# Kernel tuning notes

Hardware: AMD Instinct MI355X
Metric: run time of the kernel (lower is better)

The kernel has to match this reference:

```python
import jax, jax.numpy as jnp
import numpy as np
import math

D_MODEL, D_FF, N_EXPERTS, TOP_K, N_SHARED = 1024, 4096, 8, 2, 1
B, T = 4, 1024
SCALE = 1.0 / math.sqrt(N_SHARED + TOP_K / N_EXPERTS)


def setup_inputs() -> dict:
    key = jax.random.key(0)
    ks = jax.random.split(key, 10)
    s1 = 1.0 / math.sqrt(D_MODEL)
    s2 = 1.0 / math.sqrt(D_FF)
    return {
        "x": jax.random.normal(ks[0], (B, T, D_MODEL), dtype=jnp.float32),
        "w_router": jax.random.normal(ks[1], (N_EXPERTS, D_MODEL), dtype=jnp.float32) * s1,
        "W1": jax.random.normal(ks[2], (N_EXPERTS, D_FF, D_MODEL), dtype=jnp.float32) * s1,
        "b1": jax.random.normal(ks[3], (N_EXPERTS, D_FF), dtype=jnp.float32) * 0.02,
        "W2": jax.random.normal(ks[4], (N_EXPERTS, D_MODEL, D_FF), dtype=jnp.float32) * s2,
        "b2": jax.random.normal(ks[5], (N_EXPERTS, D_MODEL), dtype=jnp.float32) * 0.02,
        "Ws1": jax.random.normal(ks[6], (D_FF, D_MODEL), dtype=jnp.float32) * s1,
        "bs1": jax.random.normal(ks[7], (D_FF,), dtype=jnp.float32) * 0.02,
        "Ws2": jax.random.normal(ks[8], (D_MODEL, D_FF), dtype=jnp.float32) * s2,
        "bs2": jax.random.normal(ks[9], (D_MODEL,), dtype=jnp.float32) * 0.02,
    }


def reference(x, w_router, W1, b1, W2, b2, Ws1, bs1, Ws2, bs2):
    # Router: logits -> softmax -> top-k gate values (no renormalization, matching source)
    logits = jnp.einsum("btd,ed->bte", x, w_router)      # [B,T,E]
    probs = jax.nn.softmax(logits, axis=-1)
    vals, idx = jax.lax.top_k(probs, TOP_K)               # [B,T,K]
    # Scatter top-k gate values into dense per-expert gates [B,T,E]
    gates = jnp.sum(jax.nn.one_hot(idx, N_EXPERTS, dtype=x.dtype) * vals[..., None], axis=-2)

    # Shared (always-on) expert FFN
    hs = jax.nn.gelu(jnp.einsum("btd,fd->btf", x, Ws1) + bs1)
    acc = jnp.einsum("btf,df->btd", hs, Ws2) + bs2

    # Routed experts, densified combine: sum_e gate[b,t,e] * FFN_e(x[b,t])
    h = jax.nn.gelu(jnp.einsum("btd,efd->btef", x, W1) + b1)   # [B,T,E,F]
    y = jnp.einsum("btef,edf->bted", h, W2) + b2               # [B,T,E,D]
    acc = acc + jnp.einsum("bted,bte->btd", y, gates)

    return SCALE * acc
```

## Files before the change

kernel.cpp:

```cpp
#include <hip/hip_runtime.h>
#include <hip/hip_bf16.h>

#define NTOK 4096
#define DM   1024
#define DF   4096
#define ROWS_TOTAL 12288
#define BM 128
#define BN 128
#define BK 64
#define TILES_MAX 112
#define SCALE_F 0.8944271909999159f

typedef __attribute__((ext_vector_type(8))) short short8;
typedef __attribute__((ext_vector_type(4))) float floatx4;

#define GLD16(gp, lp) __builtin_amdgcn_global_load_lds( \
    (const __attribute__((address_space(1))) void*)(gp), \
    (__attribute__((address_space(3))) void*)(lp), 16, 0, 0)

__device__ __forceinline__ ushort f2bf(float f){
    __hip_bfloat16 h = __float2bfloat16(f);
    return *reinterpret_cast<ushort*>(&h);
}

__device__ __forceinline__ float gelu_tanh(float x){
    float u = 0.7978845608028654f * (x + 0.044715f * x * x * x);
    return 0.5f * x * (1.0f + tanhf(u));
}

__global__ __launch_bounds__(256) void cvt_kernel(const float* __restrict__ src,
                                                  ushort* __restrict__ dst, int n4){
    int i = blockIdx.x * 256 + threadIdx.x;
    if (i < n4){
        float4 v = reinterpret_cast<const float4*>(src)[i];
        ushort4 o = { f2bf(v.x), f2bf(v.y), f2bf(v.z), f2bf(v.w) };
        reinterpret_cast<ushort4*>(dst)[i] = o;
    }
}

__global__ __launch_bounds__(256) void router_kernel(
    const float* __restrict__ x, const float* __restrict__ wr,
    int* __restrict__ counts, int* __restrict__ te, float* __restrict__ tg,
    int* __restrict__ tokarr)
{
    const int token = blockIdx.x * 4 + (threadIdx.x >> 6);
    const int lane  = threadIdx.x & 63;
    const float* xp = x + (size_t)token * DM;
    float s[8];
    #pragma unroll
    for (int e = 0; e < 8; e++) s[e] = 0.f;
    for (int d = lane; d < DM; d += 64){
        float xv = xp[d];
        #pragma unroll
        for (int e = 0; e < 8; e++) s[e] += xv * wr[e * DM + d];
    }
    #pragma unroll
    for (int e = 0; e < 8; e++){
        float v = s[e];
        #pragma unroll
        for (int off = 32; off > 0; off >>= 1) v += __shfl_down(v, off);
        s[e] = v;
    }
    if (lane == 0){
        float m = s[0];
        #pragma unroll
        for (int e = 1; e < 8; e++) m = fmaxf(m, s[e]);
        float p[8]; float sum = 0.f;
        #pragma unroll
        for (int e = 0; e < 8; e++){ p[e] = __expf(s[e] - m); sum += p[e]; }
        float inv = 1.f / sum;
        #pragma unroll
        for (int e = 0; e < 8; e++) p[e] *= inv;
        int i1 = 0; float p1 = p[0];
        #pragma unroll
        for (int e = 1; e < 8; e++) if (p[e] > p1){ p1 = p[e]; i1 = e; }
        int i2 = -1; float p2 = -1.f;
        #pragma unroll
        for (int e = 0; e < 8; e++) if (e != i1 && p[e] > p2){ p2 = p[e]; i2 = e; }
        atomicAdd(&counts[i1], 1);
        atomicAdd(&counts[i2], 1);
        te[token*2+0] = i1; te[token*2+1] = i2;
        tg[token*2+0] = p1; tg[token*2+1] = p2;
        tokarr[token] = token;
    }
}

__global__ void scan_kernel(int* counts, int* rowbase, int* cursor, int* tiles){
    if (threadIdx.x == 0 && blockIdx.x == 0){
        int off = NTOK;
        for (int e = 0; e < 8; e++){ rowbase[e] = off; cursor[e] = off; off += counts[e]; }
        rowbase[8] = 0;
        counts[8]  = NTOK;
        int idx = 0;
        for (int e = 0; e < 9; e++){
            int c = counts[e];
            for (int mt = 0; mt * BM < c && idx < TILES_MAX; mt++)
                tiles[idx++] = (e << 8) | mt;
        }
        for (; idx < TILES_MAX; idx++) tiles[idx] = -1;
    }
}

__global__ __launch_bounds__(256) void fill_kernel(
    const int* __restrict__ te, int* cursor, int* tokarr, int* rowof)
{
    int token = blockIdx.x * 256 + threadIdx.x;
    #pragma unroll
    for (int j = 0; j < 2; j++){
        int e = te[token*2+j];
        int p = atomicAdd(&cursor[e], 1);
        tokarr[p] = token;
        rowof[token*2+j] = p;
    }
}

template<int MODE>
__global__ __launch_bounds__(256) void gemm_kernel(
    const ushort* __restrict__ Abase,
    const ushort* __restrict__ Wb, const ushort* __restrict__ Wsb,
    const float* __restrict__ brout, const float* __restrict__ bsh,
    const int* __restrict__ counts, const int* __restrict__ rowbase,
    const int* __restrict__ tokarr, const int* __restrict__ tiles,
    ushort* __restrict__ Hout, float* __restrict__ Yout)
{
    const int tile = tiles[blockIdx.x];
    if (tile < 0) return;
    const int e  = tile >> 8;
    const int mt = tile & 255;
    const int nt = blockIdx.y;
    const int cnt  = counts[e];
    const int base = rowbase[e];
    const int K = (MODE == 0) ? DM : DF;
    const int N = (MODE == 0) ? DF : DM;
    const ushort* Bp  = (e < 8) ? (Wb + (size_t)e * DF * DM) : Wsb;
    const float* bias = (e < 8) ? (brout + e * N) : bsh;

    __shared__ ushort As[BM * BK];
    __shared__ ushort Bs[BN * BK];

    const int t    = threadIdx.x;
    const int lane = t & 63;
    const int wv   = t >> 6;
    const int wm   = (wv >> 1) * 64;
    const int wn   = (wv & 1) * 64;
    const int lrow = lane & 15;
    const int quad = lane >> 4;
    const int swz8 = ((lane & 7) ^ (lane >> 3)) * 8;

    const ushort* Ap[4];
    const ushort* Bpp[4];
    ushort* Alds[4];
    ushort* Blds[4];
    #pragma unroll
    for (int i = 0; i < 4; i++){
        int rin = wv * 32 + i * 8 + (lane >> 3);
        int pos = mt * BM + rin;
        int clp = (pos < cnt) ? pos : (cnt - 1);
        if (MODE == 0) Ap[i] = Abase + (size_t)tokarr[base + clp] * DM + swz8;
        else           Ap[i] = Abase + (size_t)(base + clp) * DF + swz8;
        Bpp[i]  = Bp + (size_t)(nt * BN + rin) * K + swz8;
        Alds[i] = &As[(wv * 32 + i * 8) * BK];
        Blds[i] = &Bs[(wv * 32 + i * 8) * BK];
    }

    floatx4 acc[4][4];
    #pragma unroll
    for (int mi = 0; mi < 4; mi++)
        #pragma unroll
        for (int ni = 0; ni < 4; ni++)
            acc[mi][ni] = (floatx4){0.f, 0.f, 0.f, 0.f};

    for (int k0 = 0; k0 < K; k0 += BK){
        __syncthreads();
        #pragma unroll
        for (int i = 0; i < 4; i++){
            GLD16(Ap[i]  + k0, Alds[i]);
            GLD16(Bpp[i] + k0, Blds[i]);
        }
        __syncthreads();
        #pragma unroll
        for (int kk = 0; kk < BK; kk += 32){
            short8 af[4], bfr[4];
            #pragma unroll
            for (int mi = 0; mi < 4; mi++){
                int row  = wm + mi * 16 + lrow;
                int phys = ((kk >> 3) + quad) ^ (row & 7);
                af[mi] = *reinterpret_cast<const short8*>(&As[row * BK + phys * 8]);
            }
            #pragma unroll
            for (int ni = 0; ni < 4; ni++){
                int row  = wn + ni * 16 + lrow;
                int phys = ((kk >> 3) + quad) ^ (row & 7);
                bfr[ni] = *reinterpret_cast<const short8*>(&Bs[row * BK + phys * 8]);
            }
            #pragma unroll
            for (int mi = 0; mi < 4; mi++)
                #pragma unroll
                for (int ni = 0; ni < 4; ni++)
                    acc[mi][ni] = __builtin_amdgcn_mfma_f32_16x16x32_bf16(af[mi], bfr[ni], acc[mi][ni], 0, 0, 0);
        }
    }

    float bv[4];
    #pragma unroll
    for (int ni = 0; ni < 4; ni++) bv[ni] = bias[nt * BN + wn + ni*16 + lrow];

    #pragma unroll
    for (int mi = 0; mi < 4; mi++){
        #pragma unroll
        for (int r = 0; r < 4; r++){
            int s   = wm + mi*16 + quad*4 + r;
            int pos = mt * BM + s;
            if (pos >= cnt) continue;
            int rr = base + pos;
            if (MODE == 0){
                ushort* hp = Hout + (size_t)rr * DF + nt * BN;
                #pragma unroll
                for (int ni = 0; ni < 4; ni++){
                    float v = acc[mi][ni][r] + bv[ni];
                    hp[wn + ni*16 + lrow] = f2bf(gelu_tanh(v));
                }
            } else {
                float* yp = Yout + (size_t)rr * DM + nt * BN;
                #pragma unroll
                for (int ni = 0; ni < 4; ni++)
                    yp[wn + ni*16 + lrow] = acc[mi][ni][r] + bv[ni];
            }
        }
    }
}

__global__ __launch_bounds__(256) void combine_kernel(
    const float* __restrict__ Y, const int* __restrict__ rowof,
    const float* __restrict__ tg, float* __restrict__ out)
{
    const int token = blockIdx.x;
    const int d4    = threadIdx.x;
    const float4* Y4 = reinterpret_cast<const float4*>(Y);
    int r1 = rowof[token*2+0], r2 = rowof[token*2+1];
    float g1 = tg[token*2+0],  g2 = tg[token*2+1];
    float4 a = Y4[(size_t)token * 256 + d4];
    float4 b = Y4[(size_t)r1 * 256 + d4];
    float4 c = Y4[(size_t)r2 * 256 + d4];
    float4 o;
    o.x = SCALE_F * (a.x + g1*b.x + g2*c.x);
    o.y = SCALE_F * (a.y + g1*b.y + g2*c.y);
    o.z = SCALE_F * (a.z + g1*b.z + g2*c.z);
    o.w = SCALE_F * (a.w + g1*b.w + g2*c.w);
    reinterpret_cast<float4*>(out)[(size_t)token * 256 + d4] = o;
}

extern "C" void kernel_launch(void* const* d_in, const int* in_sizes, int n_in,
                              void* d_out, int out_size, void* d_ws, size_t ws_size,
                              hipStream_t stream) {
    const float* x   = (const float*)d_in[0];
    const float* wr  = (const float*)d_in[1];
    const float* W1  = (const float*)d_in[2];
    const float* b1  = (const float*)d_in[3];
    const float* W2  = (const float*)d_in[4];
    const float* b2  = (const float*)d_in[5];
    const float* Ws1 = (const float*)d_in[6];
    const float* bs1 = (const float*)d_in[7];
    const float* Ws2 = (const float*)d_in[8];
    const float* bs2 = (const float*)d_in[9];
    float* out = (float*)d_out;

    char* ws = (char*)d_ws;
    size_t off = 0;
    auto wsalloc = [&](size_t bytes) -> char* {
        char* p = ws + off;
        off += (bytes + 255) & ~(size_t)255;
        return p;
    };
    ushort* xb   = (ushort*)wsalloc((size_t)NTOK * DM * 2);
    ushort* w1b  = (ushort*)wsalloc((size_t)8 * DF * DM * 2);
    ushort* w2b  = (ushort*)wsalloc((size_t)8 * DM * DF * 2);
    ushort* ws1b = (ushort*)wsalloc((size_t)DF * DM * 2);
    ushort* ws2b = (ushort*)wsalloc((size_t)DM * DF * 2);
    ushort* H    = (ushort*)wsalloc((size_t)ROWS_TOTAL * DF * 2);
    int*    tokarr = (int*)wsalloc(ROWS_TOTAL * 4);
    int*    rowof  = (int*)wsalloc(NTOK * 2 * 4);
    int*    te     = (int*)wsalloc(NTOK * 2 * 4);
    float*  tg     = (float*)wsalloc(NTOK * 2 * 4);
    int*    counts = (int*)wsalloc(16 * 4);
    int*    rowbase= (int*)wsalloc(16 * 4);
    int*    cursor = (int*)wsalloc(16 * 4);
    int*    tiles  = (int*)wsalloc(TILES_MAX * 4);
    float*  Y = (float*)w1b;

    hipMemsetAsync(counts, 0, 16 * 4, stream);

    cvt_kernel<<<(NTOK*DM/4 + 255)/256, 256, 0, stream>>>(x,   xb,   NTOK*DM/4);
    cvt_kernel<<<(8*DF*DM/4 + 255)/256, 256, 0, stream>>>(W1,  w1b,  8*DF*DM/4);
    cvt_kernel<<<(8*DM*DF/4 + 255)/256, 256, 0, stream>>>(W2,  w2b,  8*DM*DF/4);
    cvt_kernel<<<(DF*DM/4   + 255)/256, 256, 0, stream>>>(Ws1, ws1b, DF*DM/4);
    cvt_kernel<<<(DM*DF/4   + 255)/256, 256, 0, stream>>>(Ws2, ws2b, DM*DF/4);

    router_kernel<<<NTOK/4, 256, 0, stream>>>(x, wr, counts, te, tg, tokarr);
    scan_kernel<<<1, 1, 0, stream>>>(counts, rowbase, cursor, tiles);
    fill_kernel<<<NTOK/256, 256, 0, stream>>>(te, cursor, tokarr, rowof);

    gemm_kernel<0><<<dim3(TILES_MAX, DF/BN), 256, 0, stream>>>(xb, w1b, ws1b, b1, bs1,
        counts, rowbase, tokarr, tiles, H, Y);
    gemm_kernel<1><<<dim3(TILES_MAX, DM/BN), 256, 0, stream>>>(H, w2b, ws2b, b2, bs2,
        counts, rowbase, tokarr, tiles, H, Y);

    combine_kernel<<<NTOK, 256, 0, stream>>>(Y, rowof, tg, out);
}
```

Before: 886.6 us.

## Fuse conversion and planning kernels, remap GEMM tiles for XCD weight locality

All five fp32-to-bf16 conversions now run in one launch, and the router/scan/fill stages become a single-block plan kernel that uses shared-memory atomics and writes a compact meta array. The GEMM grids become 1D, and each block derives its expert, M tile and N tile so that blocks sharing an N column are placed on the same XCD (blockIdx & 7), which should improve L2 reuse of weight tiles. GELU tanh is rewritten as x*sigmoid via __expf to make it cheaper. The risks are the serial single-block planning step and a fixed PMAX grid that may launch many idle blocks.

```diff
diff --git a/kernel.cpp b/kernel.cpp
--- a/kernel.cpp
+++ b/kernel.cpp
@@ -8,8 +8,8 @@
 #define BM 128
 #define BN 128
 #define BK 64
-#define TILES_MAX 112
 #define SCALE_F 0.8944271909999159f
+#define PMAX 103
 
 typedef __attribute__((ext_vector_type(8))) short short8;
 typedef __attribute__((ext_vector_type(4))) float floatx4;
@@ -23,25 +23,38 @@
     return *reinterpret_cast<ushort*>(&h);
 }
 
-__device__ __forceinline__ float gelu_tanh(float x){
-    float u = 0.7978845608028654f * (x + 0.044715f * x * x * x);
-    return 0.5f * x * (1.0f + tanhf(u));
-}
-
-__global__ __launch_bounds__(256) void cvt_kernel(const float* __restrict__ src,
-                                                  ushort* __restrict__ dst, int n4){
-    int i = blockIdx.x * 256 + threadIdx.x;
-    if (i < n4){
-        float4 v = reinterpret_cast<const float4*>(src)[i];
-        ushort4 o = { f2bf(v.x), f2bf(v.y), f2bf(v.z), f2bf(v.w) };
-        reinterpret_cast<ushort4*>(dst)[i] = o;
-    }
+__device__ __forceinline__ float gelu_tanh(float v){
+    float u2 = -1.5957691216057308f * (v + 0.044715f * v * v * v);
+    return v / (1.0f + __expf(u2));
+}
+
+#define CVT_N0 1048576u
+#define CVT_N1 9437184u
+#define CVT_N2 17825792u
+#define CVT_N3 18874368u
+#define CVT_N4 19922944u
+__global__ __launch_bounds__(256) void cvt_all(
+    const float* __restrict__ x,  const float* __restrict__ W1,
+    const float* __restrict__ W2, const float* __restrict__ Ws1,
+    const float* __restrict__ Ws2,
+    ushort* __restrict__ xb,  ushort* __restrict__ w1b, ushort* __restrict__ w2b,
+    ushort* __restrict__ ws1b, ushort* __restrict__ ws2b)
+{
+    unsigned i = blockIdx.x * 256u + threadIdx.x;
+    const float* s; ushort* d; unsigned off;
+    if      (i < CVT_N0){ s = x;   d = xb;   off = i; }
+    else if (i < CVT_N1){ s = W1;  d = w1b;  off = i - CVT_N0; }
+    else if (i < CVT_N2){ s = W2;  d = w2b;  off = i - CVT_N1; }
+    else if (i < CVT_N3){ s = Ws1; d = ws1b; off = i - CVT_N2; }
+    else                { s = Ws2; d = ws2b; off = i - CVT_N3; }
+    float4 v = reinterpret_cast<const float4*>(s)[off];
+    ushort4 o = { f2bf(v.x), f2bf(v.y), f2bf(v.z), f2bf(v.w) };
+    reinterpret_cast<ushort4*>(d)[off] = o;
 }
 
 __global__ __launch_bounds__(256) void router_kernel(
     const float* __restrict__ x, const float* __restrict__ wr,
-    int* __restrict__ counts, int* __restrict__ te, float* __restrict__ tg,
-    int* __restrict__ tokarr)
+    int* __restrict__ te, float* __restrict__ tg, int* __restrict__ tokarr)
 {
     const int token = blockIdx.x * 4 + (threadIdx.x >> 6);
     const int lane  = threadIdx.x & 63;
@@ -77,40 +90,41 @@
         int i2 = -1; float p2 = -1.f;
         #pragma unroll
         for (int e = 0; e < 8; e++) if (e != i1 && p[e] > p2){ p2 = p[e]; i2 = e; }
-        atomicAdd(&counts[i1], 1);
-        atomicAdd(&counts[i2], 1);
         te[token*2+0] = i1; te[token*2+1] = i2;
         tg[token*2+0] = p1; tg[token*2+1] = p2;
         tokarr[token] = token;
     }
 }
 
-__global__ void scan_kernel(int* counts, int* rowbase, int* cursor, int* tiles){
-    if (threadIdx.x == 0 && blockIdx.x == 0){
+__global__ __launch_bounds__(256) void plan_kernel(
+    const int* __restrict__ te, int* __restrict__ tokarr,
+    int* __restrict__ rowof, int* __restrict__ meta)
+{
+    __shared__ int lc[9], lcur[9];
+    const int t = threadIdx.x;
+    if (t < 9) lc[t] = 0;
+    __syncthreads();
+    for (int j = t; j < NTOK*2; j += 256) atomicAdd(&lc[te[j]], 1);
+    __syncthreads();
+    if (t == 0){
         int off = NTOK;
-        for (int e = 0; e < 8; e++){ rowbase[e] = off; cursor[e] = off; off += counts[e]; }
-        rowbase[8] = 0;
-        counts[8]  = NTOK;
-        int idx = 0;
-        for (int e = 0; e < 9; e++){
-            int c = counts[e];
-            for (int mt = 0; mt * BM < c && idx < TILES_MAX; mt++)
-                tiles[idx++] = (e << 8) | mt;
+        for (int e = 0; e < 8; e++){
+            lcur[e]    = off;
+            meta[e]    = lc[e];
+            meta[16+e] = off;
+            meta[32+e] = (lc[e] + BM - 1) / BM;
+            off += lc[e];
         }
-        for (; idx < TILES_MAX; idx++) tiles[idx] = -1;
-    }
-}
-
-__global__ __launch_bounds__(256) void fill_kernel(
-    const int* __restrict__ te, int* cursor, int* tokarr, int* rowof)
-{
-    int token = blockIdx.x * 256 + threadIdx.x;
-    #pragma unroll
-    for (int j = 0; j < 2; j++){
-        int e = te[token*2+j];
-        int p = atomicAdd(&cursor[e], 1);
-        tokarr[p] = token;
-        rowof[token*2+j] = p;
+        meta[8]    = NTOK;
+        meta[16+8] = 0;
+        meta[32+8] = NTOK / BM;
+    }
+    __syncthreads();
+    for (int j = t; j < NTOK*2; j += 256){
+        int e = te[j];
+        int p = atomicAdd(&lcur[e], 1);
+        tokarr[p] = j >> 1;
+        rowof[j]  = p;
     }
 }
 
@@ -119,17 +133,29 @@
     const ushort* __restrict__ Abase,
     const ushort* __restrict__ Wb, const ushort* __restrict__ Wsb,
     const float* __restrict__ brout, const float* __restrict__ bsh,
-    const int* __restrict__ counts, const int* __restrict__ rowbase,
-    const int* __restrict__ tokarr, const int* __restrict__ tiles,
+    const int* __restrict__ meta, const int* __restrict__ tokarr,
     ushort* __restrict__ Hout, float* __restrict__ Yout)
 {
-    const int tile = tiles[blockIdx.x];
-    if (tile < 0) return;
-    const int e  = tile >> 8;
-    const int mt = tile & 255;
-    const int nt = blockIdx.y;
-    const int cnt  = counts[e];
-    const int base = rowbase[e];
+    const int xcd = blockIdx.x & 7;
+    const int q   = blockIdx.x >> 3;
+    const int NTG = (MODE == 0) ? 4 : 1;
+
+    int e = -1, r = 0, a0 = 0;
+    #pragma unroll
+    for (int ee = 0; ee < 9; ee++){
+        int w = NTG * meta[32 + ee];
+        if (e < 0 && q < a0 + w){ e = ee; r = q - a0; }
+        a0 += w;
+    }
+    if (e < 0) return;
+    const int mt_e = meta[32 + e];
+    int ntg, mti;
+    if (MODE == 0){ ntg = r / mt_e; mti = r - ntg * mt_e; }
+    else          { ntg = 0;        mti = r; }
+    const int nt   = (MODE == 0) ? (xcd + 8 * ntg) : xcd;
+    const int cnt  = meta[e];
+    const int base = meta[16 + e];
+
     const int K = (MODE == 0) ? DM : DF;
     const int N = (MODE == 0) ? DF : DM;
     const ushort* Bp  = (e < 8) ? (Wb + (size_t)e * DF * DM) : Wsb;
@@ -154,7 +180,7 @@
     #pragma unroll
     for (int i = 0; i < 4; i++){
         int rin = wv * 32 + i * 8 + (lane >> 3);
-        int pos = mt * BM + rin;
+        int pos = mti * BM + rin;
         int clp = (pos < cnt) ? pos : (cnt - 1);
         if (MODE == 0) Ap[i] = Abase + (size_t)tokarr[base + clp] * DM + swz8;
         else           Ap[i] = Abase + (size_t)(base + clp) * DF + swz8;
@@ -208,23 +234,23 @@
     #pragma unroll
     for (int mi = 0; mi < 4; mi++){
         #pragma unroll
-        for (int r = 0; r < 4; r++){
-            int s   = wm + mi*16 + quad*4 + r;
-            int pos = mt * BM + s;
+        for (int rg = 0; rg < 4; rg++){
+            int s   = wm + mi*16 + quad*4 + rg;
+            int pos = mti * BM + s;
             if (pos >= cnt) continue;
             int rr = base + pos;
             if (MODE == 0){
                 ushort* hp = Hout + (size_t)rr * DF + nt * BN;
                 #pragma unroll
                 for (int ni = 0; ni < 4; ni++){
-                    float v = acc[mi][ni][r] + bv[ni];
+                    float v = acc[mi][ni][rg] + bv[ni];
                     hp[wn + ni*16 + lrow] = f2bf(gelu_tanh(v));
                 }
             } else {
                 float* yp = Yout + (size_t)rr * DM + nt * BN;
                 #pragma unroll
                 for (int ni = 0; ni < 4; ni++)
-                    yp[wn + ni*16 + lrow] = acc[mi][ni][r] + bv[ni];
+                    yp[wn + ni*16 + lrow] = acc[mi][ni][rg] + bv[ni];
             }
         }
     }
@@ -282,28 +308,18 @@
     int*    rowof  = (int*)wsalloc(NTOK * 2 * 4);
     int*    te     = (int*)wsalloc(NTOK * 2 * 4);
     float*  tg     = (float*)wsalloc(NTOK * 2 * 4);
-    int*    counts = (int*)wsalloc(16 * 4);
-    int*    rowbase= (int*)wsalloc(16 * 4);
-    int*    cursor = (int*)wsalloc(16 * 4);
-    int*    tiles  = (int*)wsalloc(TILES_MAX * 4);
+    int*    meta   = (int*)wsalloc(64 * 4);
     float*  Y = (float*)w1b;
 
-    hipMemsetAsync(counts, 0, 16 * 4, stream);
-
-    cvt_kernel<<<(NTOK*DM/4 + 255)/256, 256, 0, stream>>>(x,   xb,   NTOK*DM/4);
-    cvt_kernel<<<(8*DF*DM/4 + 255)/256, 256, 0, stream>>>(W1,  w1b,  8*DF*DM/4);
-    cvt_kernel<<<(8*DM*DF/4 + 255)/256, 256, 0, stream>>>(W2,  w2b,  8*DM*DF/4);
-    cvt_kernel<<<(DF*DM/4   + 255)/256, 256, 0, stream>>>(Ws1, ws1b, DF*DM/4);
-    cvt_kernel<<<(DM*DF/4   + 255)/256, 256, 0, stream>>>(Ws2, ws2b, DM*DF/4);
-
-    router_kernel<<<NTOK/4, 256, 0, stream>>>(x, wr, counts, te, tg, tokarr);
-    scan_kernel<<<1, 1, 0, stream>>>(counts, rowbase, cursor, tiles);
-    fill_kernel<<<NTOK/256, 256, 0, stream>>>(te, cursor, tokarr, rowof);
-
-    gemm_kernel<0><<<dim3(TILES_MAX, DF/BN), 256, 0, stream>>>(xb, w1b, ws1b, b1, bs1,
-        counts, rowbase, tokarr, tiles, H, Y);
-    gemm_kernel<1><<<dim3(TILES_MAX, DM/BN), 256, 0, stream>>>(H, w2b, ws2b, b2, bs2,
-        counts, rowbase, tokarr, tiles, H, Y);
+    cvt_all<<<CVT_N4/256, 256, 0, stream>>>(x, W1, W2, Ws1, Ws2,
+                                            xb, w1b, w2b, ws1b, ws2b);
+    router_kernel<<<NTOK/4, 256, 0, stream>>>(x, wr, te, tg, tokarr);
+    plan_kernel<<<1, 256, 0, stream>>>(te, tokarr, rowof, meta);
+
+    gemm_kernel<0><<<8 * 4 * PMAX, 256, 0, stream>>>(xb, w1b, ws1b, b1, bs1,
+        meta, tokarr, H, Y);
+    gemm_kernel<1><<<8 * PMAX, 256, 0, stream>>>(H, w2b, ws2b, b2, bs2,
+        meta, tokarr, H, Y);
 
     combine_kernel<<<NTOK, 256, 0, stream>>>(Y, rowof, tg, out);
 }
```

After: 722.1 us. 1.23x faster.
